# Performance work log

Hardware: AMD Instinct MI355X
Metric: run time of the kernel (lower is better)

Reference implementation:

```python
import jax, jax.numpy as jnp
import numpy as np

B, S, D_MODEL, H = 2, 2048, 1024, 16
DEPTH = D_MODEL // H


def setup_inputs() -> dict:
    key = jax.random.key(0)
    ks = jax.random.split(key, 12)
    s = 1.0 / np.sqrt(D_MODEL)
    inp = {
        "q": jax.random.normal(ks[0], (B, S, D_MODEL), jnp.float32),
        "k": jax.random.normal(ks[1], (B, S, D_MODEL), jnp.float32),
        "v": jax.random.normal(ks[2], (B, S, D_MODEL), jnp.float32),
        # CTRL-style causal mask: 1 where position is disallowed (future), 0 otherwise
        "mask": jnp.triu(jnp.ones((S, S), jnp.float32), k=1),
        "Wq_w": jax.random.normal(ks[3], (D_MODEL, D_MODEL), jnp.float32) * s,
        "Wq_b": jax.random.normal(ks[4], (D_MODEL,), jnp.float32) * s,
        "Wk_w": jax.random.normal(ks[5], (D_MODEL, D_MODEL), jnp.float32) * s,
        "Wk_b": jax.random.normal(ks[6], (D_MODEL,), jnp.float32) * s,
        "Wv_w": jax.random.normal(ks[7], (D_MODEL, D_MODEL), jnp.float32) * s,
        "Wv_b": jax.random.normal(ks[8], (D_MODEL,), jnp.float32) * s,
        "dense_w": jax.random.normal(ks[9], (D_MODEL, D_MODEL), jnp.float32) * s,
        "dense_b": jax.random.normal(ks[10], (D_MODEL,), jnp.float32) * s,
    }
    return inp


def _split_heads(x):
    # [B, S, D] -> [B, H, S, depth]
    b, s, _ = x.shape
    return x.reshape(b, s, H, DEPTH).transpose(0, 2, 1, 3)


def reference(q, k, v, mask, Wq_w, Wq_b, Wk_w, Wk_b, Wv_w, Wv_b, dense_w, dense_b):
    b = q.shape[0]
    # torch Linear: y = x @ W^T + b
    qh = _split_heads(q @ Wq_w.T + Wq_b)  # [B,H,Sq,dh]
    kh = _split_heads(k @ Wk_w.T + Wk_b)  # [B,H,Sk,dh]
    vh = _split_heads(v @ Wv_w.T + Wv_b)  # [B,H,Sk,dh]

    scale = 1.0 / np.sqrt(DEPTH)
    logits = jnp.einsum("bhqd,bhkd->bhqk", qh, kh) * scale  # [B,H,Sq,Sk]
    nd, ns = logits.shape[-2], logits.shape[-1]
    logits = logits + mask[ns - nd:ns, :ns] * -10000.0
    attn = jax.nn.softmax(logits, axis=-1)
    ctx = jnp.einsum("bhqk,bhkd->bhqd", attn, vh)  # [B,H,Sq,dh]
    ctx = ctx.transpose(0, 2, 1, 3).reshape(b, -1, D_MODEL)  # [B,Sq,D]
    out = ctx @ dense_w.T + dense_b
    return out
```

## Files before the change

### kernel.cpp

```cpp
#include <hip/hip_runtime.h>
#include <hip/hip_bf16.h>

typedef __bf16 bf16x8 __attribute__((ext_vector_type(8)));
typedef __bf16 bf16x4 __attribute__((ext_vector_type(4)));
typedef float  f32x4  __attribute__((ext_vector_type(4)));

#define D_MODEL 1024
#define SEQ     2048
#define NH      16
#define DH      64
#define MTOT    4096

__device__ __forceinline__ void gload16(const void* gp, void* lp) {
  __builtin_amdgcn_global_load_lds(
      (const __attribute__((address_space(1))) unsigned int*)gp,
      (__attribute__((address_space(3))) unsigned int*)lp,
      16, 0, 0);
}

struct CvtSegs {
  const float* s[7];
  __bf16*      d[7];
  int          n8[7];
};

__global__ __launch_bounds__(256) void cvt_kernel(CvtSegs c) {
  const int seg = blockIdx.y;
  const float4* s = (const float4*)c.s[seg];
  bf16x8*       d = (bf16x8*)c.d[seg];
  const int n8 = c.n8[seg];
  for (int i = blockIdx.x * 256 + threadIdx.x; i < n8; i += gridDim.x * 256) {
    float4 a = s[2 * i];
    float4 b = s[2 * i + 1];
    bf16x8 o;
    o[0] = (__bf16)a.x; o[1] = (__bf16)a.y; o[2] = (__bf16)a.z; o[3] = (__bf16)a.w;
    o[4] = (__bf16)b.x; o[5] = (__bf16)b.y; o[6] = (__bf16)b.z; o[7] = (__bf16)b.w;
    d[i] = o;
  }
}

template <int EPI>
__device__ __forceinline__ void gemm_core(const __bf16* __restrict__ A,
                                          const __bf16* __restrict__ W,
                                          const float* __restrict__ bias,
                                          void* __restrict__ outp,
                                          __bf16* Asm, __bf16* Bsm,
                                          int row0, int col0) {
  const int tid = threadIdx.x;
  const int lane = tid & 63;
  const int w = tid >> 6;
  const int lr = lane & 15, lg = lane >> 4;
  const int wr = w >> 1, wc = w & 1;
  char* AsB = (char*)Asm;
  char* BsB = (char*)Bsm;

  f32x4 acc[4][4];
#pragma unroll
  for (int i = 0; i < 4; ++i)
#pragma unroll
    for (int j = 0; j < 4; ++j) acc[i][j] = (f32x4){0.f, 0.f, 0.f, 0.f};

  for (int k0 = 0; k0 < D_MODEL; k0 += 64) {
#pragma unroll
    for (int i = 0; i < 4; ++i) {
      const int c0 = i * 4 + w;
      const int bo = c0 * 1024 + lane * 16;
      const int row = bo >> 7;
      const int gch = ((bo >> 4) & 7) ^ (row & 7);
      gload16(A + (size_t)(row0 + row) * D_MODEL + k0 + gch * 8, AsB + c0 * 1024);
      gload16(W + (size_t)(col0 + row) * D_MODEL + k0 + gch * 8, BsB + c0 * 1024);
    }
    __syncthreads();
#pragma unroll
    for (int kk = 0; kk < 2; ++kk) {
      bf16x8 af[4], bfr[4];
      const int kc = kk * 4 + lg;
#pragma unroll
      for (int mi = 0; mi < 4; ++mi) {
        const int row = wr * 64 + mi * 16 + lr;
        af[mi] = *(const bf16x8*)(AsB + row * 128 + ((kc ^ (row & 7)) << 4));
      }
#pragma unroll
      for (int ni = 0; ni < 4; ++ni) {
        const int col = wc * 64 + ni * 16 + lr;
        bfr[ni] = *(const bf16x8*)(BsB + col * 128 + ((kc ^ (col & 7)) << 4));
      }
#pragma unroll
      for (int mi = 0; mi < 4; ++mi)
#pragma unroll
        for (int ni = 0; ni < 4; ++ni)
          acc[mi][ni] = __builtin_amdgcn_mfma_f32_16x16x32_bf16(af[mi], bfr[ni],
                                                                acc[mi][ni], 0, 0, 0);
    }
    __syncthreads();
  }

#pragma unroll
  for (int mi = 0; mi < 4; ++mi) {
#pragma unroll
    for (int ni = 0; ni < 4; ++ni) {
      const int n = col0 + wc * 64 + ni * 16 + lr;
      const float bv = bias[n];
#pragma unroll
      for (int j = 0; j < 4; ++j) {
        const int m = row0 + wr * 64 + mi * 16 + lg * 4 + j;
        const float v = acc[mi][ni][j] + bv;
        if (EPI == 0) {
          __bf16* o = (__bf16*)outp;
          o[(size_t)((m >> 11) * NH + (n >> 6)) * (SEQ * DH) +
            (size_t)(m & 2047) * DH + (n & 63)] = (__bf16)v;
        } else {
          float* o = (float*)outp;
          o[(size_t)m * D_MODEL + n] = v;
        }
      }
    }
  }
}

struct QkvPtrs {
  const __bf16* A[3];
  const __bf16* W[3];
  const float*  b[3];
  __bf16*       o[3];
};

__global__ __launch_bounds__(256) void gemm_qkv_kernel(QkvPtrs p) {
  __shared__ __bf16 As[128 * 64];
  __shared__ __bf16 Bs[128 * 64];
  const int z = blockIdx.z;
  gemm_core<0>(p.A[z], p.W[z], p.b[z], p.o[z], As, Bs,
               blockIdx.x * 128, blockIdx.y * 128);
}

__global__ __launch_bounds__(256) void gemm_out_kernel(const __bf16* __restrict__ A,
                                                       const __bf16* __restrict__ W,
                                                       const float* __restrict__ b,
                                                       float* __restrict__ o) {
  __shared__ __bf16 As[128 * 64];
  __shared__ __bf16 Bs[128 * 64];
  gemm_core<1>(A, W, b, o, As, Bs, blockIdx.x * 128, blockIdx.y * 128);
}

__global__ __launch_bounds__(512, 4) void attn_kernel(const __bf16* __restrict__ qh,
                                                      const __bf16* __restrict__ kh,
                                                      const __bf16* __restrict__ vh,
                                                      __bf16* __restrict__ ctx) {
  __shared__ __bf16 Ks[2][64 * 64];
  __shared__ __bf16 Vt[2][64 * 64];
  __shared__ __bf16 Ps[8][16 * 64];

  const int bh = blockIdx.x;
  const int z  = blockIdx.y;
  const int qb = (z < 8) ? z : (23 - z);
  const int tid = threadIdx.x, lane = tid & 63, w = tid >> 6;
  const int lr = lane & 15, lg = lane >> 4;
  const size_t hoff = (size_t)bh * SEQ * DH;
  const __bf16* Q  = qh + hoff;
  const __bf16* Kp = kh + hoff;
  const __bf16* Vp = vh + hoff;
  const int q0 = qb * 128 + w * 16;

  bf16x8 qf[2];
#pragma unroll
  for (int ki = 0; ki < 2; ++ki)
    qf[ki] = *(const bf16x8*)(Q + (size_t)(q0 + lr) * DH + ki * 32 + lg * 8);

  f32x4 o[4];
#pragma unroll
  for (int ni = 0; ni < 4; ++ni) o[ni] = (f32x4){0.f, 0.f, 0.f, 0.f};
  float lsum = 0.f;

  char* Psw = (char*)Ps[w];
  const int krow = tid >> 3;
  const int kgch = (tid & 7) ^ (krow & 7);
  const int vkv  = tid & 63;
  const int vd0  = (tid >> 6) * 8;
  const int nt = 2 * (qb + 1);

  gload16(Kp + (size_t)krow * DH + kgch * 8, (char*)Ks[0] + w * 1024);
  {
    bf16x8 vv = *(const bf16x8*)(Vp + (size_t)vkv * DH + vd0);
#pragma unroll
    for (int i = 0; i < 8; ++i) {
      const int d = vd0 + i;
      Vt[0][d * 64 + ((((vkv >> 3) ^ (d & 7)) << 3) | (vkv & 7))] = vv[i];
    }
  }

  int cur = 0;
  for (int t = 0; t < nt; ++t) {
    __syncthreads();
    if (t + 1 < nt) {
      const int nxt = cur ^ 1;
      gload16(Kp + (size_t)((t + 1) * 64 + krow) * DH + kgch * 8,
              (char*)Ks[nxt] + w * 1024);
      bf16x8 vv = *(const bf16x8*)(Vp + (size_t)((t + 1) * 64 + vkv) * DH + vd0);
#pragma unroll
      for (int i = 0; i < 8; ++i) {
        const int d = vd0 + i;
        Vt[nxt][d * 64 + ((((vkv >> 3) ^ (d & 7)) << 3) | (vkv & 7))] = vv[i];
      }
    }
    if (t * 64 <= q0 + 15) {
      char* KsB = (char*)Ks[cur];
      char* VtB = (char*)Vt[cur];

      f32x4 st[4];
#pragma unroll
      for (int ni = 0; ni < 4; ++ni) st[ni] = (f32x4){0.f, 0.f, 0.f, 0.f};
      __builtin_amdgcn_s_setprio(1);
#pragma unroll
      for (int ki = 0; ki < 2; ++ki) {
        const int kc = ki * 4 + lg;
#pragma unroll
        for (int ni = 0; ni < 4; ++ni) {
          const int row = ni * 16 + lr;
          bf16x8 kf = *(const bf16x8*)(KsB + row * 128 + ((kc ^ (row & 7)) << 4));
          st[ni] = __builtin_amdgcn_mfma_f32_16x16x32_bf16(kf, qf[ki], st[ni], 0, 0, 0);
        }
      }
      __builtin_amdgcn_s_setprio(0);

      const int kvb = t * 64;
      const bool needmask = (kvb + 63 > q0);
      const int q = q0 + lr;
      float p[4][4];
      float psum = 0.f;
#pragma unroll
      for (int ni = 0; ni < 4; ++ni) {
#pragma unroll
        for (int j = 0; j < 4; ++j) {
          float v = st[ni][j] * 0.18033688f;
          if (needmask && (kvb + ni * 16 + lg * 4 + j > q)) v = -1e9f;
          const float pe = exp2f(v);
          p[ni][j] = pe;
          psum += pe;
        }
      }
      psum += __shfl_xor(psum, 16, 64);
      psum += __shfl_xor(psum, 32, 64);
      lsum += psum;

#pragma unroll
      for (int ni = 0; ni < 4; ++ni) {
        bf16x4 pk;
#pragma unroll
        for (int j = 0; j < 4; ++j) pk[j] = (__bf16)p[ni][j];
        const int chunk = 2 * ni + (lg >> 1);
        *(bf16x4*)(Psw + lr * 128 + ((chunk ^ (lr & 7)) << 4) + (lg & 1) * 8) = pk;
      }
      asm volatile("s_waitcnt lgkmcnt(0)" ::: "memory");
      __builtin_amdgcn_sched_barrier(0);

      __builtin_amdgcn_s_setprio(1);
#pragma unroll
      for (int ki = 0; ki < 2; ++ki) {
        const int kc = ki * 4 + lg;
        bf16x8 pf = *(const bf16x8*)(Psw + lr * 128 + ((kc ^ (lr & 7)) << 4));
#pragma unroll
        for (int ni = 0; ni < 4; ++ni) {
          const int d = ni * 16 + lr;
          bf16x8 vf = *(const bf16x8*)(VtB + d * 128 + ((kc ^ (lr & 7)) << 4));
          o[ni] = __builtin_amdgcn_mfma_f32_16x16x32_bf16(pf, vf, o[ni], 0, 0, 0);
        }
      }
      __builtin_amdgcn_s_setprio(0);
    }
    cur ^= 1;
  }

  const int bb = bh >> 4, hh = bh & 15;
#pragma unroll
  for (int j = 0; j < 4; ++j) {
    const int row = lg * 4 + j;
    const float inv = 1.0f / __shfl(lsum, row, 64);
    const int qrow = q0 + row;
    __bf16* orow = ctx + (size_t)(bb * SEQ + qrow) * D_MODEL + hh * DH;
#pragma unroll
    for (int ni = 0; ni < 4; ++ni)
      orow[ni * 16 + lr] = (__bf16)(o[ni][j] * inv);
  }
}

extern "C" void kernel_launch(void* const* d_in, const int* in_sizes, int n_in,
                              void* d_out, int out_size, void* d_ws, size_t ws_size,
                              hipStream_t stream) {
  (void)in_sizes; (void)n_in; (void)out_size; (void)ws_size;
  const float* q  = (const float*)d_in[0];
  const float* k  = (const float*)d_in[1];
  const float* v  = (const float*)d_in[2];
  const float* Wq = (const float*)d_in[4];
  const float* bq = (const float*)d_in[5];
  const float* Wk = (const float*)d_in[6];
  const float* bk = (const float*)d_in[7];
  const float* Wv = (const float*)d_in[8];
  const float* bv = (const float*)d_in[9];
  const float* Wd = (const float*)d_in[10];
  const float* bd = (const float*)d_in[11];

  char* ws = (char*)d_ws;
  __bf16* qb  = (__bf16*)(ws + 0);
  __bf16* kb  = (__bf16*)(ws + 8388608);
  __bf16* vb  = (__bf16*)(ws + 16777216);
  __bf16* wqb = (__bf16*)(ws + 25165824);
  __bf16* wkb = (__bf16*)(ws + 27262976);
  __bf16* wvb = (__bf16*)(ws + 29360128);
  __bf16* wdb = (__bf16*)(ws + 31457280);
  __bf16* qhp = (__bf16*)(ws + 33554432);
  __bf16* khp = (__bf16*)(ws + 41943040);
  __bf16* vhp = (__bf16*)(ws + 50331648);
  __bf16* ctxp= (__bf16*)(ws + 58720256);

  CvtSegs cs;
  cs.s[0] = q;  cs.d[0] = qb;  cs.n8[0] = 524288;
  cs.s[1] = k;  cs.d[1] = kb;  cs.n8[1] = 524288;
  cs.s[2] = v;  cs.d[2] = vb;  cs.n8[2] = 524288;
  cs.s[3] = Wq; cs.d[3] = wqb; cs.n8[3] = 131072;
  cs.s[4] = Wk; cs.d[4] = wkb; cs.n8[4] = 131072;
  cs.s[5] = Wv; cs.d[5] = wvb; cs.n8[5] = 131072;
  cs.s[6] = Wd; cs.d[6] = wdb; cs.n8[6] = 131072;
  cvt_kernel<<<dim3(256, 7, 1), dim3(256), 0, stream>>>(cs);

  QkvPtrs qp;
  qp.A[0] = qb;  qp.A[1] = kb;  qp.A[2] = vb;
  qp.W[0] = wqb; qp.W[1] = wkb; qp.W[2] = wvb;
  qp.b[0] = bq;  qp.b[1] = bk;  qp.b[2] = bv;
  qp.o[0] = qhp; qp.o[1] = khp; qp.o[2] = vhp;
  gemm_qkv_kernel<<<dim3(32, 8, 3), dim3(256), 0, stream>>>(qp);

  attn_kernel<<<dim3(32, 16, 1), dim3(512), 0, stream>>>(qhp, khp, vhp, ctxp);

  gemm_out_kernel<<<dim3(32, 8, 1), dim3(256), 0, stream>>>(ctxp, wdb, bd, (float*)d_out);
}
```

Measured before the change: 140.5 us.

## Use 4-wave attention blocks with strided query rows across the sequence

```diff
diff --git a/kernel.cpp b/kernel.cpp
--- a/kernel.cpp
+++ b/kernel.cpp
@@ -142,24 +142,23 @@
   gemm_core<1>(A, W, b, o, As, Bs, blockIdx.x * 128, blockIdx.y * 128);
 }
 
-__global__ __launch_bounds__(512, 4) void attn_kernel(const __bf16* __restrict__ qh,
+__global__ __launch_bounds__(256, 4) void attn_kernel(const __bf16* __restrict__ qh,
                                                       const __bf16* __restrict__ kh,
                                                       const __bf16* __restrict__ vh,
                                                       __bf16* __restrict__ ctx) {
   __shared__ __bf16 Ks[2][64 * 64];
   __shared__ __bf16 Vt[2][64 * 64];
-  __shared__ __bf16 Ps[8][16 * 64];
+  __shared__ __bf16 Ps[4][16 * 64];
 
   const int bh = blockIdx.x;
-  const int z  = blockIdx.y;
-  const int qb = (z < 8) ? z : (23 - z);
+  const int zb = 31 - blockIdx.y;
   const int tid = threadIdx.x, lane = tid & 63, w = tid >> 6;
   const int lr = lane & 15, lg = lane >> 4;
   const size_t hoff = (size_t)bh * SEQ * DH;
   const __bf16* Q  = qh + hoff;
   const __bf16* Kp = kh + hoff;
   const __bf16* Vp = vh + hoff;
-  const int q0 = qb * 128 + w * 16;
+  const int q0 = (zb + w * 32) * 16;
 
   bf16x8 qf[2];
 #pragma unroll
@@ -172,18 +171,24 @@
   float lsum = 0.f;
 
   char* Psw = (char*)Ps[w];
-  const int krow = tid >> 3;
-  const int kgch = (tid & 7) ^ (krow & 7);
-  const int vkv  = tid & 63;
-  const int vd0  = (tid >> 6) * 8;
-  const int nt = 2 * (qb + 1);
-
-  gload16(Kp + (size_t)krow * DH + kgch * 8, (char*)Ks[0] + w * 1024);
-  {
-    bf16x8 vv = *(const bf16x8*)(Vp + (size_t)vkv * DH + vd0);
+  const int vkv = tid & 63;
+  const int vd0 = (tid >> 6) * 8;
+  const int nt = ((zb * 16 + 1551) >> 6) + 1;
+
+#pragma unroll
+  for (int s = 0; s < 2; ++s) {
+    const int c = (w * 2 + s) * 64 + lane;
+    const int row = c >> 3;
+    const int gch = (c & 7) ^ (row & 7);
+    gload16(Kp + (size_t)row * DH + gch * 8, (char*)Ks[0] + (w * 2 + s) * 1024);
+  }
+#pragma unroll
+  for (int s = 0; s < 2; ++s) {
+    const int d0 = vd0 + s * 32;
+    bf16x8 vv = *(const bf16x8*)(Vp + (size_t)vkv * DH + d0);
 #pragma unroll
     for (int i = 0; i < 8; ++i) {
-      const int d = vd0 + i;
+      const int d = d0 + i;
       Vt[0][d * 64 + ((((vkv >> 3) ^ (d & 7)) << 3) | (vkv & 7))] = vv[i];
     }
   }
@@ -193,13 +198,23 @@
     __syncthreads();
     if (t + 1 < nt) {
       const int nxt = cur ^ 1;
-      gload16(Kp + (size_t)((t + 1) * 64 + krow) * DH + kgch * 8,
-              (char*)Ks[nxt] + w * 1024);
-      bf16x8 vv = *(const bf16x8*)(Vp + (size_t)((t + 1) * 64 + vkv) * DH + vd0);
-#pragma unroll
-      for (int i = 0; i < 8; ++i) {
-        const int d = vd0 + i;
-        Vt[nxt][d * 64 + ((((vkv >> 3) ^ (d & 7)) << 3) | (vkv & 7))] = vv[i];
+#pragma unroll
+      for (int s = 0; s < 2; ++s) {
+        const int c = (w * 2 + s) * 64 + lane;
+        const int row = c >> 3;
+        const int gch = (c & 7) ^ (row & 7);
+        gload16(Kp + (size_t)((t + 1) * 64 + row) * DH + gch * 8,
+                (char*)Ks[nxt] + (w * 2 + s) * 1024);
+      }
+#pragma unroll
+      for (int s = 0; s < 2; ++s) {
+        const int d0 = vd0 + s * 32;
+        bf16x8 vv = *(const bf16x8*)(Vp + (size_t)((t + 1) * 64 + vkv) * DH + d0);
+#pragma unroll
+        for (int i = 0; i < 8; ++i) {
+          const int d = d0 + i;
+          Vt[nxt][d * 64 + ((((vkv >> 3) ^ (d & 7)) << 3) | (vkv & 7))] = vv[i];
+        }
       }
     }
     if (t * 64 <= q0 + 15) {
@@ -329,7 +344,7 @@
   qp.o[0] = qhp; qp.o[1] = khp; qp.o[2] = vhp;
   gemm_qkv_kernel<<<dim3(32, 8, 3), dim3(256), 0, stream>>>(qp);
 
-  attn_kernel<<<dim3(32, 16, 1), dim3(512), 0, stream>>>(qhp, khp, vhp, ctxp);
+  attn_kernel<<<dim3(32, 32, 1), dim3(256), 0, stream>>>(qhp, khp, vhp, ctxp);
 
   gemm_out_kernel<<<dim3(32, 8, 1), dim3(256), 0, stream>>>(ctxp, wdb, bd, (float*)d_out);
 }
```

Result: no change. 138.3 us (-1.6%).
